# Kernel optimization log

Measured on AMD Instinct MI355X. Metric: run time of the kernel, lower is better.

The kernel has to match this reference:

```python
import jax, jax.numpy as jnp
import numpy as np

B, LQ, LA, H = 32, 1024, 1024, 512
NEG_INF = jnp.float32(-1e7)  # matches torch masked_fill_(-10000000.0)


def setup_inputs() -> dict:
    key = jax.random.key(0)
    k1, k2, k3, k4 = jax.random.split(key, 4)
    q = jax.random.normal(k1, (B, LQ, H), dtype=jnp.float32)
    a = jax.random.normal(k2, (B, LA, H), dtype=jnp.float32)
    q_mask = jax.random.randint(k3, (B, LQ, 1), 0, 2).astype(jnp.int32)
    a_mask = jax.random.randint(k4, (B, LA, 1), 0, 2).astype(jnp.int32)
    # learned scalar, initialized exactly as in __init__
    temperature = jnp.float32(1.0 / np.sqrt(H))
    return {"q": q, "a": a, "q_mask": q_mask, "a_mask": a_mask,
            "temperature": temperature}


def reference(q, a, q_mask, a_mask, temperature):
    # scaled co-attention scores: [B, Lq, La]
    attn = jnp.einsum('bqh,bah->bqa', q, a) * temperature
    # validity mask via outer product of per-token masks (nonzero = valid)
    mask = jnp.matmul(q_mask.astype(jnp.float32),
                      a_mask.transpose(0, 2, 1).astype(jnp.float32)) != 0
    attn = jnp.where(mask, attn, NEG_INF)
    # dual-axis softmax over the SAME score matrix
    attn_q = jax.nn.softmax(attn, axis=1)  # normalize over Lq
    attn_a = jax.nn.softmax(attn, axis=2)  # normalize over La
    # aggregation: a_s = attn_q^T @ q -> [B, La, H]; q_s = attn_a @ a -> [B, Lq, H]
    a_s = jnp.einsum('bqa,bqh->bah', attn_q, q)
    q_s = jnp.einsum('bqa,bah->bqh', attn_a, a)
    return (jnp.concatenate([q, q_s], axis=-1),
            jnp.concatenate([a, a_s], axis=-1))
```

## Files before the change

### kernel.cpp

```cpp
#include <hip/hip_runtime.h>
#include <cstdint>
#include <cstddef>

#define NB   32
#define LQA  1024
#define HD   512

typedef __attribute__((ext_vector_type(4))) float  f32x4;
typedef __attribute__((ext_vector_type(8))) short  s16x8;
typedef __attribute__((ext_vector_type(4))) unsigned short u16x4;

static __device__ __forceinline__ unsigned short f2bf(float f) {
  unsigned int u = __builtin_bit_cast(unsigned int, f);
  u += 0x7fffu + ((u >> 16) & 1u);
  return (unsigned short)(u >> 16);
}
static __device__ __forceinline__ float bf2f(unsigned short h) {
  unsigned int u = ((unsigned int)h) << 16;
  return __builtin_bit_cast(float, u);
}
static __device__ __forceinline__ u16x4 cvt4(f32x4 v) {
  u16x4 r;
  r.x = f2bf(v.x); r.y = f2bf(v.y); r.z = f2bf(v.z); r.w = f2bf(v.w);
  return r;
}

typedef __attribute__((address_space(1))) const void gas_void;
typedef __attribute__((address_space(3))) void las_void;
static __device__ __forceinline__ void gload_lds16(const void* g, void* l) {
  __builtin_amdgcn_global_load_lds((gas_void*)g, (las_void*)l, 16, 0, 0);
}

__global__ __launch_bounds__(256) void k_transpose_copy(
    const float* __restrict__ src,
    float* __restrict__ out_left,
    unsigned short* __restrict__ dstT,
    unsigned short* __restrict__ dstN)
{
  const int b  = blockIdx.z;
  const int h0 = blockIdx.x * 64;
  const int q0 = blockIdx.y * 64;
  const int t  = threadIdx.x;

  __shared__ unsigned short T[64 * 68];

  const float* sb = src + (size_t)b * LQA * HD;
  float* ob       = out_left + (size_t)b * LQA * 1024;
  unsigned short* db  = dstT + (size_t)b * HD * LQA;
  unsigned short* dbn = dstN + (size_t)b * LQA * HD;

#pragma unroll
  for (int j = 0; j < 4; ++j) {
    int f = t + 256 * j;
    int r = f >> 4;
    int c = (f & 15) * 4;
    f32x4 v = *(const f32x4*)(sb + (size_t)(q0 + r) * HD + h0 + c);
    *(f32x4*)(ob + (size_t)(q0 + r) * 1024 + h0 + c) = v;
    u16x4 cv = cvt4(v);
    *(u16x4*)&dbn[(size_t)(q0 + r) * HD + h0 + c] = cv;
    *(u16x4*)&T[r * 68 + c] = cv;
  }
  __syncthreads();
#pragma unroll
  for (int j = 0; j < 4; ++j) {
    int f = t + 256 * j;
    int orow = f >> 4;
    int c = (f & 15) * 4;
    u16x4 v;
    v.x = T[(c + 0) * 68 + orow];
    v.y = T[(c + 1) * 68 + orow];
    v.z = T[(c + 2) * 68 + orow];
    v.w = T[(c + 3) * 68 + orow];
    *(u16x4*)&db[(size_t)(h0 + orow) * LQA + q0 + c] = v;
  }
}

__global__ __launch_bounds__(256) void k_scores(
    const unsigned short* __restrict__ qb16, const unsigned short* __restrict__ ab16,
    const int* __restrict__ qmask, const int* __restrict__ amask,
    const float* __restrict__ temp_p,
    unsigned short* __restrict__ E, unsigned short* __restrict__ ET)
{
  const int b  = blockIdx.z;
  const int m0 = blockIdx.x * 128;
  const int n0 = blockIdx.y * 128;
  const int t  = threadIdx.x;
  const int lane = t & 63;
  const int w  = t >> 6;
  const int moff = (w & 1) * 64;
  const int noff = (w >> 1) * 64;
  const int lrow = lane & 15;
  const int quad = lane >> 4;

  __shared__ __align__(16) unsigned short smem[128 * 132];
  unsigned short* As = smem;
  unsigned short* Bs = smem + 4096;

  const unsigned short* qb = qb16 + (size_t)b * LQA * HD;
  const unsigned short* ab = ab16 + (size_t)b * LQA * HD;

  const int fa = t, fb = t + 256;
  const unsigned short* qg0 = qb + (size_t)(m0 + (fa >> 2)) * HD + (fa & 3) * 8;
  const unsigned short* qg1 = qb + (size_t)(m0 + (fb >> 2)) * HD + (fb & 3) * 8;
  const unsigned short* ag0 = ab + (size_t)(n0 + (fa >> 2)) * HD + (fa & 3) * 8;
  const unsigned short* ag1 = ab + (size_t)(n0 + (fb >> 2)) * HD + (fb & 3) * 8;
  unsigned short* As0 = As + w * 512;
  unsigned short* As1 = As + (4 + w) * 512;
  unsigned short* Bs0 = Bs + w * 512;
  unsigned short* Bs1 = Bs + (4 + w) * 512;

  f32x4 acc[4][4];
#pragma unroll
  for (int i = 0; i < 4; ++i)
#pragma unroll
    for (int j = 0; j < 4; ++j) acc[i][j] = (f32x4)0.f;

  for (int kt = 0; kt < HD / 32; ++kt) {
    const int ko = kt * 32;
    gload_lds16(qg0 + ko, As0);
    gload_lds16(qg1 + ko, As1);
    gload_lds16(ag0 + ko, Bs0);
    gload_lds16(ag1 + ko, Bs1);
    __syncthreads();
    s16x8 af[4], bfr[4];
#pragma unroll
    for (int i = 0; i < 4; ++i) {
      af[i]  = *(const s16x8*)&As[(moff + i * 16 + lrow) * 32 + quad * 8];
      bfr[i] = *(const s16x8*)&Bs[(noff + i * 16 + lrow) * 32 + quad * 8];
    }
#pragma unroll
    for (int i = 0; i < 4; ++i)
#pragma unroll
      for (int j = 0; j < 4; ++j)
        acc[i][j] = __builtin_amdgcn_mfma_f32_16x16x32_bf16(af[i], bfr[j], acc[i][j], 0, 0, 0);
    __syncthreads();
  }

  unsigned short* Cs = smem;
  const float temp = temp_p[0];
  const int* qmb = qmask + b * LQA;
  const int* amb = amask + b * LQA;
#pragma unroll
  for (int i = 0; i < 4; ++i) {
#pragma unroll
    for (int j = 0; j < 4; ++j) {
      int ncol = noff + j * 16 + lrow;
      float am = (amb[n0 + ncol] != 0) ? 1.f : 0.f;
#pragma unroll
      for (int r = 0; r < 4; ++r) {
        int mrow = moff + i * 16 + quad * 4 + r;
        float qm = (qmb[m0 + mrow] != 0) ? 1.f : 0.f;
        float e = __expf(acc[i][j][r] * temp) * am * qm;
        Cs[mrow * 132 + ncol] = f2bf(e);
      }
    }
  }
  __syncthreads();
  const size_t Ebase = (size_t)b * LQA * LQA;
#pragma unroll
  for (int jj = 0; jj < 16; ++jj) {
    int f = t + 256 * jj;
    int row = f >> 5;
    int c = (f & 31) * 4;
    u16x4 v = *(const u16x4*)&Cs[row * 132 + c];
    *(u16x4*)&E[Ebase + (size_t)(m0 + row) * LQA + n0 + c] = v;
  }
#pragma unroll
  for (int jj = 0; jj < 16; ++jj) {
    int f = t + 256 * jj;
    int orow = f >> 5;
    int c = (f & 31) * 4;
    u16x4 v;
    v.x = Cs[(c + 0) * 132 + orow];
    v.y = Cs[(c + 1) * 132 + orow];
    v.z = Cs[(c + 2) * 132 + orow];
    v.w = Cs[(c + 3) * 132 + orow];
    *(u16x4*)&ET[Ebase + (size_t)(n0 + orow) * LQA + m0 + c] = v;
  }
}

__global__ __launch_bounds__(256) void k_rowsum_stats(
    const unsigned short* __restrict__ Emat, float2* __restrict__ invadd)
{
  const int t = threadIdx.x;
  const int rowg = blockIdx.x * 16 + (t >> 4);
  const int s = t & 15;
  const unsigned short* rp = Emat + (size_t)rowg * LQA;
  float sum = 0.f;
#pragma unroll
  for (int it = 0; it < 16; ++it) {
    u16x4 v = *(const u16x4*)&rp[it * 64 + s * 4];
    sum += bf2f(v.x) + bf2f(v.y) + bf2f(v.z) + bf2f(v.w);
  }
  sum += __shfl_xor(sum, 1);
  sum += __shfl_xor(sum, 2);
  sum += __shfl_xor(sum, 4);
  sum += __shfl_xor(sum, 8);
  if (s == 0) {
    float2 o;
    if (sum > 0.f) { o.x = 1.f / sum; o.y = 0.f; }
    else           { o.x = 0.f;       o.y = 1.f / 1024.f; }
    invadd[rowg] = o;
  }
}

__global__ __launch_bounds__(256) void k_rowsum_plain(
    const unsigned short* __restrict__ M, float* __restrict__ sums)
{
  const int t = threadIdx.x;
  const int rowg = blockIdx.x * 16 + (t >> 4);
  const int s = t & 15;
  const unsigned short* rp = M + (size_t)rowg * LQA;
  float sum = 0.f;
#pragma unroll
  for (int it = 0; it < 16; ++it) {
    u16x4 v = *(const u16x4*)&rp[it * 64 + s * 4];
    sum += bf2f(v.x) + bf2f(v.y) + bf2f(v.z) + bf2f(v.w);
  }
  sum += __shfl_xor(sum, 1);
  sum += __shfl_xor(sum, 2);
  sum += __shfl_xor(sum, 4);
  sum += __shfl_xor(sum, 8);
  if (s == 0) sums[rowg] = sum;
}

__global__ __launch_bounds__(256) void k_agg(
    const unsigned short* __restrict__ Emat,
    const unsigned short* __restrict__ Bt,
    const float2* __restrict__ invadd,
    const float* __restrict__ bsum,
    float* __restrict__ outp)
{
  const int b  = blockIdx.z;
  const int m0 = blockIdx.x * 128;
  const int n0 = blockIdx.y * 128;
  const int t  = threadIdx.x;
  const int lane = t & 63;
  const int w  = t >> 6;
  const int moff = (w & 1) * 64;
  const int noff = (w >> 1) * 64;
  const int lrow = lane & 15;
  const int quad = lane >> 4;

  __shared__ __align__(16) unsigned short As[128 * 32];
  __shared__ __align__(16) unsigned short Bs[128 * 32];

  const unsigned short* Eb = Emat + (size_t)b * LQA * LQA;
  const unsigned short* Bb = Bt + (size_t)b * HD * LQA;

  const int fa = t, fb = t + 256;
  const unsigned short* eg0 = Eb + (size_t)(m0 + (fa >> 2)) * LQA + (fa & 3) * 8;
  const unsigned short* eg1 = Eb + (size_t)(m0 + (fb >> 2)) * LQA + (fb & 3) * 8;
  const unsigned short* bg0 = Bb + (size_t)(n0 + (fa >> 2)) * LQA + (fa & 3) * 8;
  const unsigned short* bg1 = Bb + (size_t)(n0 + (fb >> 2)) * LQA + (fb & 3) * 8;
  unsigned short* As0 = As + w * 512;
  unsigned short* As1 = As + (4 + w) * 512;
  unsigned short* Bs0 = Bs + w * 512;
  unsigned short* Bs1 = Bs + (4 + w) * 512;

  f32x4 acc[4][4];
#pragma unroll
  for (int i = 0; i < 4; ++i)
#pragma unroll
    for (int j = 0; j < 4; ++j) acc[i][j] = (f32x4)0.f;

  for (int kt = 0; kt < LQA / 32; ++kt) {
    const int ko = kt * 32;
    gload_lds16(eg0 + ko, As0);
    gload_lds16(eg1 + ko, As1);
    gload_lds16(bg0 + ko, Bs0);
    gload_lds16(bg1 + ko, Bs1);
    __syncthreads();
    s16x8 af[4], bfr[4];
#pragma unroll
    for (int i = 0; i < 4; ++i) {
      af[i]  = *(const s16x8*)&As[(moff + i * 16 + lrow) * 32 + quad * 8];
      bfr[i] = *(const s16x8*)&Bs[(noff + i * 16 + lrow) * 32 + quad * 8];
    }
#pragma unroll
    for (int i = 0; i < 4; ++i)
#pragma unroll
      for (int j = 0; j < 4; ++j)
        acc[i][j] = __builtin_amdgcn_mfma_f32_16x16x32_bf16(af[i], bfr[j], acc[i][j], 0, 0, 0);
    __syncthreads();
  }

  const float2* ia = invadd + b * LQA;
  const float* bs = bsum + b * HD;
  float* ob = outp + (size_t)b * LQA * 1024;
#pragma unroll
  for (int i = 0; i < 4; ++i) {
#pragma unroll
    for (int j = 0; j < 4; ++j) {
      int ncol = noff + j * 16 + lrow;
      float bsv = bs[n0 + ncol];
#pragma unroll
      for (int r = 0; r < 4; ++r) {
        int mrow = moff + i * 16 + quad * 4 + r;
        float2 v = ia[m0 + mrow];
        ob[(size_t)(m0 + mrow) * 1024 + 512 + n0 + ncol] =
            v.x * acc[i][j][r] + v.y * bsv;
      }
    }
  }
}

extern "C" void kernel_launch(void* const* d_in, const int* in_sizes, int n_in,
                              void* d_out, int out_size, void* d_ws, size_t ws_size,
                              hipStream_t stream) {
  (void)in_sizes; (void)n_in; (void)out_size; (void)ws_size;
  const float* q    = (const float*)d_in[0];
  const float* a    = (const float*)d_in[1];
  const int*   qm   = (const int*)d_in[2];
  const int*   am   = (const int*)d_in[3];
  const float* temp = (const float*)d_in[4];

  float* out0 = (float*)d_out;
  float* out1 = out0 + (size_t)NB * LQA * 1024;

  char* ws = (char*)d_ws;
  const size_t MB = 1024ull * 1024ull;
  unsigned short* E    = (unsigned short*)(ws);
  unsigned short* ET   = (unsigned short*)(ws + 64 * MB);
  unsigned short* qT   = (unsigned short*)(ws + 128 * MB);
  unsigned short* aT   = (unsigned short*)(ws + 160 * MB);
  unsigned short* qb16 = (unsigned short*)(ws + 192 * MB);
  unsigned short* ab16 = (unsigned short*)(ws + 224 * MB);
  float2* invq = (float2*)(ws + 256 * MB);
  float2* inva = (float2*)(ws + 256 * MB + 262144);
  float*  qsum = (float*)(ws + 256 * MB + 524288);
  float*  asum = (float*)(ws + 256 * MB + 524288 + 65536);

  k_transpose_copy<<<dim3(8, 16, NB), 256, 0, stream>>>(q, out0, qT, qb16);
  k_transpose_copy<<<dim3(8, 16, NB), 256, 0, stream>>>(a, out1, aT, ab16);
  k_rowsum_plain<<<dim3(NB * HD / 16), 256, 0, stream>>>(qT, qsum);
  k_rowsum_plain<<<dim3(NB * HD / 16), 256, 0, stream>>>(aT, asum);
  k_scores<<<dim3(8, 8, NB), 256, 0, stream>>>(qb16, ab16, qm, am, temp, E, ET);
  k_rowsum_stats<<<dim3(NB * LQA / 16), 256, 0, stream>>>(E, invq);
  k_rowsum_stats<<<dim3(NB * LQA / 16), 256, 0, stream>>>(ET, inva);
  k_agg<<<dim3(8, 4, NB), 256, 0, stream>>>(E,  aT, invq, asum, out0);
  k_agg<<<dim3(8, 4, NB), 256, 0, stream>>>(ET, qT, inva, qsum, out1);
}
```

Baseline: 628.2 us.

## Fuse row/column sum reductions into prep and scores kernels via atomics

Merges the two transpose-copy launches into one prep kernel that also computes the per-column sums of q and a with shuffle reductions and atomics, which removes the separate rowsum_plain passes over the transposed copies. The scores kernel now accumulates the row and column sums of the exponentiated scores in registers and atomically adds them. This drops the two rowsum_stats kernels that reread E and ET, and the aggregation kernel computes the reciprocal itself. The scores epilogue is split into two phases to fit both E and ET staging in shared memory, and a memset is added to zero the accumulators. The cost is atomic contention, sums taken from fp32 values rather than the rounded bf16 ones, and an extra sync phase.

After: 638.6 us. No clear change (+1.7%).

```diff
diff --git a/kernel.cpp b/kernel.cpp
--- a/kernel.cpp
+++ b/kernel.cpp
@@ -9,16 +9,13 @@
 typedef __attribute__((ext_vector_type(4))) float  f32x4;
 typedef __attribute__((ext_vector_type(8))) short  s16x8;
 typedef __attribute__((ext_vector_type(4))) unsigned short u16x4;
+typedef __attribute__((ext_vector_type(2))) unsigned short u16x2;
 
 static __device__ __forceinline__ unsigned short f2bf(float f) {
   unsigned int u = __builtin_bit_cast(unsigned int, f);
   u += 0x7fffu + ((u >> 16) & 1u);
   return (unsigned short)(u >> 16);
 }
-static __device__ __forceinline__ float bf2f(unsigned short h) {
-  unsigned int u = ((unsigned int)h) << 16;
-  return __builtin_bit_cast(float, u);
-}
 static __device__ __forceinline__ u16x4 cvt4(f32x4 v) {
   u16x4 r;
   r.x = f2bf(v.x); r.y = f2bf(v.y); r.z = f2bf(v.z); r.w = f2bf(v.w);
@@ -31,47 +28,73 @@
   __builtin_amdgcn_global_load_lds((gas_void*)g, (las_void*)l, 16, 0, 0);
 }
 
-__global__ __launch_bounds__(256) void k_transpose_copy(
-    const float* __restrict__ src,
-    float* __restrict__ out_left,
-    unsigned short* __restrict__ dstT,
-    unsigned short* __restrict__ dstN)
+__global__ __launch_bounds__(256) void k_prep(
+    const float* __restrict__ qsrc, const float* __restrict__ asrc,
+    float* __restrict__ out0, float* __restrict__ out1,
+    unsigned short* __restrict__ qT, unsigned short* __restrict__ aT,
+    unsigned short* __restrict__ qb16, unsigned short* __restrict__ ab16,
+    float* __restrict__ qsum, float* __restrict__ asum)
 {
-  const int b  = blockIdx.z;
+  const int which = blockIdx.z >> 5;
+  const int b  = blockIdx.z & 31;
   const int h0 = blockIdx.x * 64;
   const int q0 = blockIdx.y * 64;
   const int t  = threadIdx.x;
-
-  __shared__ unsigned short T[64 * 68];
+  const int lane = t & 63;
+
+  const float* src = which ? asrc : qsrc;
+  float* out_left  = which ? out1 : out0;
+  unsigned short* dstT = which ? aT : qT;
+  unsigned short* dstN = which ? ab16 : qb16;
+  float* sums          = which ? asum : qsum;
+
+  __shared__ unsigned short T[64 * 66];
 
   const float* sb = src + (size_t)b * LQA * HD;
   float* ob       = out_left + (size_t)b * LQA * 1024;
   unsigned short* db  = dstT + (size_t)b * HD * LQA;
   unsigned short* dbn = dstN + (size_t)b * LQA * HD;
 
+  const int c = (t & 15) * 4;
+  f32x4 csum = (f32x4)0.f;
+
 #pragma unroll
   for (int j = 0; j < 4; ++j) {
-    int f = t + 256 * j;
-    int r = f >> 4;
-    int c = (f & 15) * 4;
+    int r = (t >> 4) + 16 * j;
     f32x4 v = *(const f32x4*)(sb + (size_t)(q0 + r) * HD + h0 + c);
     *(f32x4*)(ob + (size_t)(q0 + r) * 1024 + h0 + c) = v;
     u16x4 cv = cvt4(v);
     *(u16x4*)&dbn[(size_t)(q0 + r) * HD + h0 + c] = cv;
-    *(u16x4*)&T[r * 68 + c] = cv;
+    T[(c + 0) * 66 + r] = cv.x;
+    T[(c + 1) * 66 + r] = cv.y;
+    T[(c + 2) * 66 + r] = cv.z;
+    T[(c + 3) * 66 + r] = cv.w;
+    csum += v;
+  }
+#pragma unroll
+  for (int k = 16; k <= 32; k <<= 1) {
+    csum.x += __shfl_xor(csum.x, k);
+    csum.y += __shfl_xor(csum.y, k);
+    csum.z += __shfl_xor(csum.z, k);
+    csum.w += __shfl_xor(csum.w, k);
+  }
+  if ((lane >> 4) == 0) {
+    float* sp = sums + b * HD + h0 + c;
+    atomicAdd(sp + 0, csum.x);
+    atomicAdd(sp + 1, csum.y);
+    atomicAdd(sp + 2, csum.z);
+    atomicAdd(sp + 3, csum.w);
   }
   __syncthreads();
 #pragma unroll
   for (int j = 0; j < 4; ++j) {
     int f = t + 256 * j;
     int orow = f >> 4;
-    int c = (f & 15) * 4;
-    u16x4 v;
-    v.x = T[(c + 0) * 68 + orow];
-    v.y = T[(c + 1) * 68 + orow];
-    v.z = T[(c + 2) * 68 + orow];
-    v.w = T[(c + 3) * 68 + orow];
-    *(u16x4*)&db[(size_t)(h0 + orow) * LQA + q0 + c] = v;
+    int cq = (f & 15) * 4;
+    u16x2 lo = *(const u16x2*)&T[orow * 66 + cq];
+    u16x2 hi = *(const u16x2*)&T[orow * 66 + cq + 2];
+    u16x4 v; v.x = lo.x; v.y = lo.y; v.z = hi.x; v.w = hi.y;
+    *(u16x4*)&db[(size_t)(h0 + orow) * LQA + q0 + cq] = v;
   }
 }
 
@@ -79,7 +102,8 @@
     const unsigned short* __restrict__ qb16, const unsigned short* __restrict__ ab16,
     const int* __restrict__ qmask, const int* __restrict__ amask,
     const float* __restrict__ temp_p,
-    unsigned short* __restrict__ E, unsigned short* __restrict__ ET)
+    unsigned short* __restrict__ E, unsigned short* __restrict__ ET,
+    float* __restrict__ sumEq, float* __restrict__ sumEa)
 {
   const int b  = blockIdx.z;
   const int m0 = blockIdx.x * 128;
@@ -92,9 +116,11 @@
   const int lrow = lane & 15;
   const int quad = lane >> 4;
 
-  __shared__ __align__(16) unsigned short smem[128 * 132];
+  __shared__ __align__(16) unsigned short smem[8704 + 8448];
   unsigned short* As = smem;
   unsigned short* Bs = smem + 4096;
+  unsigned short* Cs_h  = smem;
+  unsigned short* CsT_h = smem + 8704;
 
   const unsigned short* qb = qb16 + (size_t)b * LQA * HD;
   const unsigned short* ab = ab16 + (size_t)b * LQA * HD;
@@ -136,98 +162,95 @@
     __syncthreads();
   }
 
-  unsigned short* Cs = smem;
   const float temp = temp_p[0];
   const int* qmb = qmask + b * LQA;
   const int* amb = amask + b * LQA;
-#pragma unroll
-  for (int i = 0; i < 4; ++i) {
-#pragma unroll
-    for (int j = 0; j < 4; ++j) {
-      int ncol = noff + j * 16 + lrow;
-      float am = (amb[n0 + ncol] != 0) ? 1.f : 0.f;
-#pragma unroll
-      for (int r = 0; r < 4; ++r) {
-        int mrow = moff + i * 16 + quad * 4 + r;
-        float qm = (qmb[m0 + mrow] != 0) ? 1.f : 0.f;
-        float e = __expf(acc[i][j][r] * temp) * am * qm;
-        Cs[mrow * 132 + ncol] = f2bf(e);
-      }
-    }
-  }
-  __syncthreads();
+  float amv[4], qmv[4][4];
+#pragma unroll
+  for (int j = 0; j < 4; ++j)
+    amv[j] = (amb[n0 + noff + j * 16 + lrow] != 0) ? 1.f : 0.f;
+#pragma unroll
+  for (int i = 0; i < 4; ++i)
+#pragma unroll
+    for (int r = 0; r < 4; ++r)
+      qmv[i][r] = (qmb[m0 + moff + i * 16 + quad * 4 + r] != 0) ? 1.f : 0.f;
+
+#pragma unroll
+  for (int i = 0; i < 4; ++i)
+#pragma unroll
+    for (int j = 0; j < 4; ++j)
+#pragma unroll
+      for (int r = 0; r < 4; ++r)
+        acc[i][j][r] = __expf(acc[i][j][r] * temp) * amv[j] * qmv[i][r];
+
+#pragma unroll
+  for (int i = 0; i < 4; ++i)
+#pragma unroll
+    for (int r = 0; r < 4; ++r) {
+      float rs = acc[i][0][r] + acc[i][1][r] + acc[i][2][r] + acc[i][3][r];
+      rs += __shfl_xor(rs, 1);
+      rs += __shfl_xor(rs, 2);
+      rs += __shfl_xor(rs, 4);
+      rs += __shfl_xor(rs, 8);
+      if (lrow == 0)
+        atomicAdd(&sumEq[b * LQA + m0 + moff + i * 16 + quad * 4 + r], rs);
+    }
+#pragma unroll
+  for (int j = 0; j < 4; ++j) {
+    float cs = 0.f;
+#pragma unroll
+    for (int i = 0; i < 4; ++i)
+#pragma unroll
+      for (int r = 0; r < 4; ++r) cs += acc[i][j][r];
+    cs += __shfl_xor(cs, 16);
+    cs += __shfl_xor(cs, 32);
+    if (quad == 0)
+      atomicAdd(&sumEa[b * LQA + n0 + noff + j * 16 + lrow], cs);
+  }
+
   const size_t Ebase = (size_t)b * LQA * LQA;
 #pragma unroll
-  for (int jj = 0; jj < 16; ++jj) {
-    int f = t + 256 * jj;
-    int row = f >> 5;
-    int c = (f & 31) * 4;
-    u16x4 v = *(const u16x4*)&Cs[row * 132 + c];
-    *(u16x4*)&E[Ebase + (size_t)(m0 + row) * LQA + n0 + c] = v;
-  }
-#pragma unroll
-  for (int jj = 0; jj < 16; ++jj) {
-    int f = t + 256 * jj;
-    int orow = f >> 5;
-    int c = (f & 31) * 4;
-    u16x4 v;
-    v.x = Cs[(c + 0) * 132 + orow];
-    v.y = Cs[(c + 1) * 132 + orow];
-    v.z = Cs[(c + 2) * 132 + orow];
-    v.w = Cs[(c + 3) * 132 + orow];
-    *(u16x4*)&ET[Ebase + (size_t)(n0 + orow) * LQA + m0 + c] = v;
-  }
-}
-
-__global__ __launch_bounds__(256) void k_rowsum_stats(
-    const unsigned short* __restrict__ Emat, float2* __restrict__ invadd)
-{
-  const int t = threadIdx.x;
-  const int rowg = blockIdx.x * 16 + (t >> 4);
-  const int s = t & 15;
-  const unsigned short* rp = Emat + (size_t)rowg * LQA;
-  float sum = 0.f;
-#pragma unroll
-  for (int it = 0; it < 16; ++it) {
-    u16x4 v = *(const u16x4*)&rp[it * 64 + s * 4];
-    sum += bf2f(v.x) + bf2f(v.y) + bf2f(v.z) + bf2f(v.w);
-  }
-  sum += __shfl_xor(sum, 1);
-  sum += __shfl_xor(sum, 2);
-  sum += __shfl_xor(sum, 4);
-  sum += __shfl_xor(sum, 8);
-  if (s == 0) {
-    float2 o;
-    if (sum > 0.f) { o.x = 1.f / sum; o.y = 0.f; }
-    else           { o.x = 0.f;       o.y = 1.f / 1024.f; }
-    invadd[rowg] = o;
-  }
-}
-
-__global__ __launch_bounds__(256) void k_rowsum_plain(
-    const unsigned short* __restrict__ M, float* __restrict__ sums)
-{
-  const int t = threadIdx.x;
-  const int rowg = blockIdx.x * 16 + (t >> 4);
-  const int s = t & 15;
-  const unsigned short* rp = M + (size_t)rowg * LQA;
-  float sum = 0.f;
-#pragma unroll
-  for (int it = 0; it < 16; ++it) {
-    u16x4 v = *(const u16x4*)&rp[it * 64 + s * 4];
-    sum += bf2f(v.x) + bf2f(v.y) + bf2f(v.z) + bf2f(v.w);
-  }
-  sum += __shfl_xor(sum, 1);
-  sum += __shfl_xor(sum, 2);
-  sum += __shfl_xor(sum, 4);
-  sum += __shfl_xor(sum, 8);
-  if (s == 0) sums[rowg] = sum;
+  for (int ph = 0; ph < 2; ++ph) {
+    if ((w >> 1) == ph) {
+#pragma unroll
+      for (int i = 0; i < 4; ++i)
+#pragma unroll
+        for (int j = 0; j < 4; ++j) {
+          int ncl = j * 16 + lrow;
+#pragma unroll
+          for (int r = 0; r < 4; ++r) {
+            int mrow = moff + i * 16 + quad * 4 + r;
+            unsigned short bv = f2bf(acc[i][j][r]);
+            Cs_h[mrow * 68 + ncl] = bv;
+            CsT_h[ncl * 132 + mrow] = bv;
+          }
+        }
+    }
+    __syncthreads();
+#pragma unroll
+    for (int jj = 0; jj < 8; ++jj) {
+      int f = t + 256 * jj;
+      int row = f >> 4;
+      int cl = (f & 15) * 4;
+      u16x4 v = *(const u16x4*)&Cs_h[row * 68 + cl];
+      *(u16x4*)&E[Ebase + (size_t)(m0 + row) * LQA + n0 + 64 * ph + cl] = v;
+    }
+#pragma unroll
+    for (int jj = 0; jj < 8; ++jj) {
+      int f = t + 256 * jj;
+      int row = f >> 5;
+      int cl = (f & 31) * 4;
+      u16x4 v = *(const u16x4*)&CsT_h[row * 132 + cl];
+      *(u16x4*)&ET[Ebase + (size_t)(n0 + 64 * ph + row) * LQA + m0 + cl] = v;
+    }
+    __syncthreads();
+  }
 }
 
 __global__ __launch_bounds__(256) void k_agg(
     const unsigned short* __restrict__ Emat,
     const unsigned short* __restrict__ Bt,
-    const float2* __restrict__ invadd,
+    const float* __restrict__ rowsum,
     const float* __restrict__ bsum,
     float* __restrict__ outp)
 {
@@ -285,7 +308,7 @@
     __syncthreads();
   }
 
-  const float2* ia = invadd + b * LQA;
+  const float* rs = rowsum + b * LQA;
   const float* bs = bsum + b * HD;
   float* ob = outp + (size_t)b * LQA * 1024;
 #pragma unroll
@@ -297,9 +320,11 @@
 #pragma unroll
       for (int r = 0; r < 4; ++r) {
         int mrow = moff + i * 16 + quad * 4 + r;
-        float2 v = ia[m0 + mrow];
+        float s = rs[m0 + mrow];
+        float inv = (s > 0.f) ? (1.f / s) : 0.f;
+        float add = (s > 0.f) ? 0.f : (1.f / 1024.f);
         ob[(size_t)(m0 + mrow) * 1024 + 512 + n0 + ncol] =
-            v.x * acc[i][j][r] + v.y * bsv;
+            inv * acc[i][j][r] + add * bsv;
       }
     }
   }
@@ -326,18 +351,17 @@
   unsigned short* aT   = (unsigned short*)(ws + 160 * MB);
   unsigned short* qb16 = (unsigned short*)(ws + 192 * MB);
   unsigned short* ab16 = (unsigned short*)(ws + 224 * MB);
-  float2* invq = (float2*)(ws + 256 * MB);
-  float2* inva = (float2*)(ws + 256 * MB + 262144);
-  float*  qsum = (float*)(ws + 256 * MB + 524288);
-  float*  asum = (float*)(ws + 256 * MB + 524288 + 65536);
-
-  k_transpose_copy<<<dim3(8, 16, NB), 256, 0, stream>>>(q, out0, qT, qb16);
-  k_transpose_copy<<<dim3(8, 16, NB), 256, 0, stream>>>(a, out1, aT, ab16);
-  k_rowsum_plain<<<dim3(NB * HD / 16), 256, 0, stream>>>(qT, qsum);
-  k_rowsum_plain<<<dim3(NB * HD / 16), 256, 0, stream>>>(aT, asum);
-  k_scores<<<dim3(8, 8, NB), 256, 0, stream>>>(qb16, ab16, qm, am, temp, E, ET);
-  k_rowsum_stats<<<dim3(NB * LQA / 16), 256, 0, stream>>>(E, invq);
-  k_rowsum_stats<<<dim3(NB * LQA / 16), 256, 0, stream>>>(ET, inva);
-  k_agg<<<dim3(8, 4, NB), 256, 0, stream>>>(E,  aT, invq, asum, out0);
-  k_agg<<<dim3(8, 4, NB), 256, 0, stream>>>(ET, qT, inva, qsum, out1);
-}
+  char* stats = ws + 256 * MB;
+  float* sumEq = (float*)(stats);
+  float* sumEa = (float*)(stats + 131072);
+  float* qsum  = (float*)(stats + 262144);
+  float* asum  = (float*)(stats + 327680);
+  hipMemsetAsync(stats, 0, 393216, stream);
+
+  k_prep<<<dim3(8, 16, 2 * NB), 256, 0, stream>>>(q, a, out0, out1, qT, aT,
+                                                  qb16, ab16, qsum, asum);
+  k_scores<<<dim3(8, 8, NB), 256, 0, stream>>>(qb16, ab16, qm, am, temp,
+                                               E, ET, sumEq, sumEa);
+  k_agg<<<dim3(8, 4, NB), 256, 0, stream>>>(E,  aT, sumEq, asum, out0);
+  k_agg<<<dim3(8, 4, NB), 256, 0, stream>>>(ET, qT, sumEa, qsum, out1);
+}
```
